# Optimization experiments

Hardware: AMD Instinct MI355X
Metric: run time of the kernel (lower is better)

## Reference

```python
import jax, jax.numpy as jnp
import numpy as np

EMBED_DIM = 1024
NUM_HEADS = 16
D_K = EMBED_DIM // NUM_HEADS
GAMMA = 1.0


def setup_inputs() -> dict:
    key = jax.random.key(0)
    ks = jax.random.split(key, 6)
    B, S, E = 4, 2048, EMBED_DIM
    scale = 1.0 / np.sqrt(E)
    x = jax.random.normal(ks[0], (B, S, E), dtype=jnp.float32)
    mask = jax.random.randint(ks[1], (B, S), 0, 2, dtype=jnp.int32)
    Wq = jax.random.normal(ks[2], (E, E), dtype=jnp.float32) * scale
    Wk = jax.random.normal(ks[3], (E, E), dtype=jnp.float32) * scale
    Wv = jax.random.normal(ks[4], (E, E), dtype=jnp.float32) * scale
    Wo = jax.random.normal(ks[5], (E, E), dtype=jnp.float32) * scale
    return {"x": x, "mask": mask, "Wq": Wq, "Wk": Wk, "Wv": Wv, "Wo": Wo}


def reference(x, mask, Wq, Wk, Wv, Wo):
    B, S, E = x.shape
    H, Dk = NUM_HEADS, D_K
    # projections (nn.Linear: y = x @ W.T), split heads -> [B, H, S, Dk]
    def proj(W):
        return (x @ W.T).reshape(B, S, H, Dk).transpose(0, 2, 1, 3)
    q = proj(Wq)
    k = proj(Wk)
    v = proj(Wv)
    # RBF kernel scores: exp(-gamma * ||q_i - k_j||^2)
    q_norm = jnp.sum(q * q, axis=-1, keepdims=True)            # [B,H,S,1]
    k_norm = jnp.sum(k * k, axis=-1, keepdims=True)            # [B,H,S,1]
    qk = jnp.einsum('bhsd,bhtd->bhst', q, k)                   # [B,H,S,S]
    dist_sq = q_norm + jnp.swapaxes(k_norm, -2, -1) - 2.0 * qk
    attn = jnp.exp(-GAMMA * dist_sq)
    # mask over keys: [B,1,1,S]
    attn = jnp.where(mask[:, None, None, :] == 0, 0.0, attn)
    # dropout is identity in eval mode
    out = jnp.einsum('bhst,bhtd->bhsd', attn, v)               # [B,H,S,Dk]
    out = out.transpose(0, 2, 1, 3).reshape(B, S, E)
    return out @ Wo.T
```

## Files before the change

kernel.cpp:

```cpp
#include <hip/hip_runtime.h>
#include <hip/hip_bf16.h>
#include <cstdint>
#include <cstddef>

#define B_ 4
#define S_ 2048
#define E_ 1024
#define H_ 16
#define BS_ (B_*S_)
#define BHS_ (B_*H_*S_)
#define MAXCAND (1u<<18)
#define SLOTS 512

static constexpr float T_SEARCH = 50.0f;
static constexpr float T_CUT    = 48.5f;

typedef __attribute__((ext_vector_type(8))) short bf16x8;
typedef __attribute__((ext_vector_type(4))) float f32x4;

static __device__ __forceinline__ unsigned short f32_to_bf16(float f){
  unsigned u = __float_as_uint(f);
  return (unsigned short)((u + 0x7fffu + ((u >> 16) & 1u)) >> 16);
}
static __device__ __forceinline__ void gload_lds16(const void* g, void* l){
  __builtin_amdgcn_global_load_lds(
      (const __attribute__((address_space(1))) unsigned int*)g,
      (__attribute__((address_space(3))) unsigned int*)l, 16, 0, 0);
}
static __device__ __forceinline__ float dot4(float4 a, float4 b){
  return a.x*b.x + a.y*b.y + a.z*b.z + a.w*b.w;
}

#define VMW(N_) asm volatile("s_waitcnt vmcnt(" #N_ ")" ::: "memory")
#define BAR()  do{ __builtin_amdgcn_s_barrier(); __builtin_amdgcn_sched_barrier(0); }while(0)

__global__ void cast_compact_k(const float* __restrict__ x,
                               const float* __restrict__ wq, const float* __restrict__ wk,
                               const int* __restrict__ mask,
                               unsigned short* __restrict__ xb, unsigned short* __restrict__ wqkb,
                               int* __restrict__ tmap, int* __restrict__ vcount){
  int blk = blockIdx.x;
  if (blk >= 5120){
    int b = blk - 5120, tid = threadIdx.x;
    __shared__ int ps[256];
    int loc[8]; int cnt = 0;
    #pragma unroll
    for (int j = 0; j < 8; ++j){ int m = mask[b*S_ + tid*8 + j]; loc[j] = m; cnt += m; }
    ps[tid] = cnt; __syncthreads();
    for (int off = 1; off < 256; off <<= 1){
      int v = (tid >= off) ? ps[tid-off] : 0;
      __syncthreads(); ps[tid] += v; __syncthreads();
    }
    int base = ps[tid] - cnt;
    #pragma unroll
    for (int j = 0; j < 8; ++j)
      if (loc[j]){ tmap[b*S_ + base] = tid*8 + j; ++base; }
    if (tid == 255) vcount[b] = ps[255];
    return;
  }
  const float* src; unsigned short* dst; int base;
  if (blk < 4096){ src = x;  dst = xb;                  base = blk; }
  else if (blk < 4608){ src = wq; dst = wqkb;           base = blk - 4096; }
  else { src = wk; dst = wqkb + (size_t)E_*E_;          base = blk - 4608; }
  size_t i = (size_t)base*256 + threadIdx.x;
  const float4* s4 = reinterpret_cast<const float4*>(src) + 2*i;
  float4 a = s4[0], b = s4[1];
  float v[8] = {a.x,a.y,a.z,a.w,b.x,b.y,b.z,b.w};
  union { unsigned short us[8]; uint4 u4; } o;
  #pragma unroll
  for (int j = 0; j < 8; ++j) o.us[j] = f32_to_bf16(v[j]);
  reinterpret_cast<uint4*>(dst)[i] = o.u4;
}

#define PROJ_STAGE(buf_, k0_) do{                                              \
  _Pragma("unroll") for (int i_ = 0; i_ < 4; ++i_){                            \
    int r_  = wave*32 + i_*8 + srow;                                           \
    int cs_ = sc ^ (r_ & 7);                                                   \
    gload_lds16(xb + ((size_t)(bb << 11) + arow[i_])*1024 + (k0_) + cs_*8,     \
                &At[buf_][(wave*32 + i_*8)*64]);                               \
    gload_lds16(Bw + (size_t)(n0 + r_)*1024 + (k0_) + cs_*8,                   \
                &Bt[buf_][(wave*32 + i_*8)*64]);                               \
  }                                                                            \
}while(0)

#define PROJ_COMPUTE(buf_) do{                                                 \
  _Pragma("unroll") for (int kk = 0; kk < 2; ++kk){                            \
    bf16x8 af[4], bf_[4];                                                      \
    _Pragma("unroll") for (int mf = 0; mf < 4; ++mf){                          \
      int r = wr*64 + mf*16 + fr;                                              \
      af[mf] = *reinterpret_cast<const bf16x8*>(                               \
          &At[buf_][r*64 + ((kk*4 + fc) ^ (r & 7))*8]);                        \
    }                                                                          \
    _Pragma("unroll") for (int nf = 0; nf < 4; ++nf){                          \
      int r = wc*64 + nf*16 + fr;                                              \
      bf_[nf] = *reinterpret_cast<const bf16x8*>(                              \
          &Bt[buf_][r*64 + ((kk*4 + fc) ^ (r & 7))*8]);                        \
    }                                                                          \
    _Pragma("unroll") for (int mf = 0; mf < 4; ++mf)                           \
    _Pragma("unroll") for (int nf = 0; nf < 4; ++nf)                           \
      acc[mf][nf] = __builtin_amdgcn_mfma_f32_16x16x32_bf16(                   \
          af[mf], bf_[nf], acc[mf][nf], 0, 0, 0);                              \
  }                                                                            \
}while(0)

__global__ __launch_bounds__(256) void proj_hm_k(
    const unsigned short* __restrict__ xb,
    const unsigned short* __restrict__ Wqkb,
    const int* __restrict__ tmap, const int* __restrict__ vcount,
    unsigned short* __restrict__ Qhm, unsigned short* __restrict__ Kc,
    float* __restrict__ qn, float* __restrict__ knc){
  const int z = blockIdx.z;
  const int m0 = blockIdx.x * 128, n0 = blockIdx.y * 128;
  const int bb = m0 >> 11, tc0 = m0 & 2047;
  const int vc = vcount[bb];
  if (z == 1 && tc0 >= vc) return;
  const unsigned short* Bw = Wqkb + (size_t)z*E_*E_;
  unsigned short* Out = z ? Kc : Qhm;
  float* Nrm = z ? knc : qn;

  __shared__ unsigned short At[2][128*64];
  __shared__ unsigned short Bt[2][128*64];
  const int tid = threadIdx.x, wave = tid >> 6, lane = tid & 63;
  const int wr = wave >> 1, wc = wave & 1;
  const int fr = lane & 15, fc = lane >> 4;
  const int srow = lane >> 3, sc = lane & 7;

  int arow[4];
  #pragma unroll
  for (int i = 0; i < 4; ++i){
    int r = wave*32 + i*8 + srow;
    int tc = tc0 + r;
    arow[i] = z ? ((tc < vc) ? tmap[bb*S_ + tc] : 0) : tc;
  }

  f32x4 acc[4][4] = {};

  PROJ_STAGE(0, 0);
  PROJ_STAGE(1, 64);
  VMW(8); BAR();
  #pragma unroll 2
  for (int t = 0; t < 16; ++t){
    PROJ_COMPUTE(t & 1);
    BAR();
    if (t + 2 < 16){
      PROJ_STAGE(t & 1, (t + 2)*64);
      VMW(8); BAR();
    } else if (t + 1 < 16){
      VMW(0); BAR();
    }
  }

  const int h = (n0 >> 6) + wc;
  const size_t rowbase = (size_t)((bb << 4) | h)*S_;
  #pragma unroll
  for (int mf = 0; mf < 4; ++mf)
    #pragma unroll
    for (int r = 0; r < 4; ++r){
      int rowb = tc0 + wr*64 + mf*16 + fc*4 + r;
      #pragma unroll
      for (int nf = 0; nf < 4; ++nf)
        Out[(rowbase + rowb)*64 + nf*16 + fr] = f32_to_bf16(acc[mf][nf][r]);
      float s = 0.f;
      #pragma unroll
      for (int nf = 0; nf < 4; ++nf) s += acc[mf][nf][r]*acc[mf][nf][r];
      s += __shfl_xor(s, 1); s += __shfl_xor(s, 2);
      s += __shfl_xor(s, 4); s += __shfl_xor(s, 8);
      if (fr == 0) Nrm[rowbase + rowb] = s;
    }
}

#define STAGE_K(slot_, c_) do{                                                 \
  _Pragma("unroll") for (int j_ = 0; j_ < 2; ++j_){                            \
    int rr_ = wave*16 + j_*8 + srow;                                           \
    gload_lds16(Kh + (size_t)((c_)*64 + rr_)*64 + (sc ^ (rr_ & 7))*8,          \
                &Kt[slot_][(wave*16 + j_*8)*64]);                              \
  }                                                                            \
}while(0)

#define TESTCHUNK(slot_, c_) do{                                               \
  int t0_ = (c_)*64;                                                           \
  bf16x8 af_[2], bfr_[4][2]; float knh_[4];                                    \
  { int r_ = wave*16 + fr;                                                     \
    _Pragma("unroll") for (int kk_ = 0; kk_ < 2; ++kk_)                        \
      af_[kk_] = *reinterpret_cast<const bf16x8*>(                             \
          &Qt[r_*64 + (((kk_*4 + fc) ^ (r_ & 7))*8)]); }                       \
  _Pragma("unroll") for (int nf_ = 0; nf_ < 4; ++nf_){                         \
    int tl_ = nf_*16 + fr;                                                     \
    _Pragma("unroll") for (int kk_ = 0; kk_ < 2; ++kk_)                        \
      bfr_[nf_][kk_] = *reinterpret_cast<const bf16x8*>(                       \
          &Kt[slot_][tl_*64 + (((kk_*4 + fc) ^ (tl_ & 7))*8)]);                \
    int t_ = t0_ + tl_;                                                        \
    knh_[nf_] = (t_ < vc) ? 0.5f*knl[t_] : 1e30f;                              \
  }                                                                            \
  f32x4 acc[4];                                                                \
  _Pragma("unroll") for (int nf_ = 0; nf_ < 4; ++nf_){                         \
    acc[nf_] = __builtin_amdgcn_mfma_f32_16x16x32_bf16(                        \
        af_[0], bfr_[nf_][0], z4, 0, 0, 0);                                    \
    acc[nf_] = __builtin_amdgcn_mfma_f32_16x16x32_bf16(                        \
        af_[1], bfr_[nf_][1], acc[nf_], 0, 0, 0);                              \
  }                                                                            \
  int hit_ = 0;                                                                \
  _Pragma("unroll") for (int nf_ = 0; nf_ < 4; ++nf_)                          \
  _Pragma("unroll") for (int r_ = 0; r_ < 4; ++r_)                             \
    hit_ |= (acc[nf_][r_] > qa[r_] + knh_[nf_]) ? 1 : 0;                       \
  if (__any(hit_)) hitmask |= (1u << (c_));                                    \
}while(0)

#define EMITCHUNK(c_) do{                                                      \
  int t0_ = (c_)*64;                                                           \
  bf16x8 af_[2], bfr_[4][2]; float knh_[4];                                    \
  { int r_ = wave*16 + fr;                                                     \
    _Pragma("unroll") for (int kk_ = 0; kk_ < 2; ++kk_)                        \
      af_[kk_] = *reinterpret_cast<const bf16x8*>(                             \
          &Qt[r_*64 + (((kk_*4 + fc) ^ (r_ & 7))*8)]); }                       \
  _Pragma("unroll") for (int nf_ = 0; nf_ < 4; ++nf_){                         \
    int tl_ = nf_*16 + fr;                                                     \
    _Pragma("unroll") for (int kk_ = 0; kk_ < 2; ++kk_)                        \
      bfr_[nf_][kk_] = *reinterpret_cast<const bf16x8*>(                       \
          Kh + (size_t)(t0_ + tl_)*64 + (kk_*4 + fc)*8);                       \
    int t_ = t0_ + tl_;                                                        \
    knh_[nf_] = (t_ < vc) ? 0.5f*knl[t_] : 1e30f;                              \
  }                                                                            \
  f32x4 acc[4];                                                                \
  _Pragma("unroll") for (int nf_ = 0; nf_ < 4; ++nf_){                         \
    acc[nf_] = __builtin_amdgcn_mfma_f32_16x16x32_bf16(                        \
        af_[0], bfr_[nf_][0], z4, 0, 0, 0);                                    \
    acc[nf_] = __builtin_amdgcn_mfma_f32_16x16x32_bf16(                        \
        af_[1], bfr_[nf_][1], acc[nf_], 0, 0, 0);                              \
  }                                                                            \
  _Pragma("unroll") for (int nf_ = 0; nf_ < 4; ++nf_)                          \
  _Pragma("unroll") for (int r_ = 0; r_ < 4; ++r_){                            \
    if (acc[nf_][r_] > qa[r_] + knh_[nf_]){                                    \
      int t_ = t0_ + nf_*16 + fr;                                              \
      if (t_ < vc){                                                            \
        int s_ = s0 + wave*16 + fc*4 + r_;                                     \
        unsigned idx_ = atomicAdd(cnt, 1u);                                    \
        if (idx_ < MAXCAND)                                                    \
          cand[idx_] = ((unsigned)b << 26) | ((unsigned)h << 22)               \
                     | ((unsigned)s_ << 11) | (unsigned)t_;                    \
        int qi_ = (bh << 11) | s_;                                             \
        if (atomicCAS((unsigned*)&qslotm[qi_], 0u, 1u) == 0u){                 \
          int sl_ = atomicAdd(&lcnt[h], 1);                                    \
          if (sl_ < SLOTS){                                                    \
            qlist[h*SLOTS + sl_] = (b << 11) | s_;                             \
            float4 zz_ = {0.f,0.f,0.f,0.f};                                    \
            float4* dz_ = reinterpret_cast<float4*>(                           \
                qex + (size_t)(h*SLOTS + sl_)*64);                             \
            for (int jz_ = 0; jz_ < 16; ++jz_) dz_[jz_] = zz_;                 \
            qslotm[qi_] = sl_ + 2;                                             \
          }                                                                    \
        }                                                                      \
        int ki_ = (bh << 11) | t_;                                             \
        if (atomicCAS((unsigned*)&kslotm[ki_], 0u, 1u) == 0u){                 \
          int sl_ = atomicAdd(&lcnt[16 + h], 1);                               \
          if (sl_ < SLOTS){                                                    \
            klist[h*SLOTS + sl_] = (b << 11) | t_;                             \
            float4 zz_ = {0.f,0.f,0.f,0.f};                                    \
            float4* d0_ = reinterpret_cast<float4*>(                           \
                kex + (size_t)(h*SLOTS + sl_)*64);                             \
            float4* d1_ = reinterpret_cast<float4*>(                           \
                vex + (size_t)(h*SLOTS + sl_)*64);                             \
            for (int jz_ = 0; jz_ < 16; ++jz_){ d0_[jz_] = zz_; d1_[jz_] = zz_; } \
            kslotm[ki_] = sl_ + 2;                                             \
          }                                                                    \
        }                                                                      \
      }                                                                        \
    }                                                                          \
  }                                                                            \
}while(0)

__global__ __launch_bounds__(256) void search_k(
    const unsigned short* __restrict__ Qhm, const unsigned short* __restrict__ Kc,
    const float* __restrict__ qn, const float* __restrict__ knc,
    const int* __restrict__ vcount,
    unsigned* __restrict__ cnt, unsigned* __restrict__ cand,
    int* __restrict__ lcnt, int* __restrict__ qlist, int* __restrict__ klist,
    int* __restrict__ qslotm, int* __restrict__ kslotm,
    float* __restrict__ qex, float* __restrict__ kex, float* __restrict__ vex){
  __shared__ unsigned short Qt[64*64];
  __shared__ unsigned short Kt[3][64*64];
  __shared__ float knl[S_];
  const int wave = threadIdx.x >> 6, lane = threadIdx.x & 63;
  const int bh = blockIdx.x & 63;
  const int s0 = (blockIdx.x >> 6) * 64;
  const int b = bh >> 4, h = bh & 15;
  const int vc = vcount[b];
  const int nt = (vc + 63) >> 6;
  if (nt == 0) return;
  const int fr = lane & 15, fc = lane >> 4;
  const int srow = lane >> 3, sc = lane & 7;
  const unsigned short* Qh = Qhm + (size_t)bh*S_*64;
  const unsigned short* Kh = Kc + (size_t)bh*S_*64;
  const float* qnb = qn + (size_t)bh*S_;
  const float* knb = knc + (size_t)bh*S_;
  const f32x4 z4 = {0.f, 0.f, 0.f, 0.f};

  float qa[4];
  #pragma unroll
  for (int r = 0; r < 4; ++r)
    qa[r] = 0.5f*(qnb[s0 + wave*16 + fc*4 + r] - T_SEARCH);
  float qamin = fminf(fminf(qa[0], qa[1]), fminf(qa[2], qa[3]));
  asm volatile("" :: "v"(qamin));
  asm volatile("s_waitcnt vmcnt(0)" ::: "memory");
  __builtin_amdgcn_sched_barrier(0);

  #pragma unroll
  for (int i = 0; i < 2; ++i){
    int r = wave*16 + i*8 + srow;
    gload_lds16(Qh + (size_t)(s0 + r)*64 + (sc ^ (r & 7))*8, &Qt[(wave*16 + i*8)*64]);
  }
  gload_lds16(knb + wave*512 + lane*4,       &knl[wave*512]);
  gload_lds16(knb + wave*512 + 256 + lane*4, &knl[wave*512 + 256]);
  STAGE_K(0, 0);
  if (nt > 1) STAGE_K(1, 1);

  unsigned hitmask = 0u;
  int c = 0, sl = 0;
  for (; c + 2 < nt; ++c){
    VMW(2); BAR();
    int sl2 = sl + 2; if (sl2 >= 3) sl2 -= 3;
    STAGE_K(sl2, c + 2);
    TESTCHUNK(sl, c);
    ++sl; if (sl == 3) sl = 0;
  }
  if (c + 1 < nt){ VMW(2); BAR(); TESTCHUNK(sl, c); ++c; ++sl; if (sl == 3) sl = 0; }
  VMW(0); BAR(); TESTCHUNK(sl, c);

  while (hitmask){
    int cc = __builtin_ctz(hitmask);
    hitmask &= hitmask - 1u;
    EMITCHUNK(cc);
  }
}

__global__ __launch_bounds__(256) void exact_rows_k(
    const float* __restrict__ x, const int* __restrict__ tmap,
    const float* __restrict__ Wq, const float* __restrict__ Wk,
    const float* __restrict__ Wv,
    const int* __restrict__ lcnt,
    const int* __restrict__ qlist, const int* __restrict__ klist,
    float* __restrict__ qex, float* __restrict__ kex, float* __restrict__ vex){
  int p = blockIdx.x, h = blockIdx.y, z = blockIdx.z;
  int R = lcnt[(z == 0 ? 0 : 16) + h]; if (R > SLOTS) R = SLOTS;
  if (R == 0) return;
  const float* W = (z == 0) ? Wq : (z == 1 ? Wk : Wv);
  const int* list = (z == 0) ? qlist : klist;
  float* dst = (z == 0) ? qex : (z == 1 ? kex : vex);
  int d = threadIdx.x >> 2, j = threadIdx.x & 3;
  const float4* w4 = reinterpret_cast<const float4*>(W + (size_t)(h*64 + d)*E_ + p*64 + j*16);
  float4 wa = w4[0], wb = w4[1], wcv = w4[2], wd = w4[3];
  for (int r = 0; r < R; ++r){
    int e = list[h*SLOTS + r];
    int b = e >> 11, rr = e & 2047;
    int row = (z == 0) ? rr : tmap[b*S_ + rr];
    const float4* x4 = reinterpret_cast<const float4*>(x + (size_t)(b*S_ + row)*E_ + p*64 + j*16);
    float acc = dot4(x4[0], wa) + dot4(x4[1], wb) + dot4(x4[2], wcv) + dot4(x4[3], wd);
    acc += __shfl_xor(acc, 1);
    acc += __shfl_xor(acc, 2);
    if (j == 0) atomicAdd(&dst[(size_t)(h*SLOTS + r)*64 + d], acc);
  }
}

__global__ __launch_bounds__(256) void d2scatter_k(
    const unsigned* __restrict__ cnt, const unsigned* __restrict__ cand,
    const int* __restrict__ qslotm, const int* __restrict__ kslotm,
    const float* __restrict__ qex, const float* __restrict__ kex,
    const float* __restrict__ vex, const float* __restrict__ Wo,
    float* __restrict__ out){
  unsigned n = *cnt; if (n > MAXCAND) n = MAXCAND;
  int lane = threadIdx.x & 63;
  for (unsigned i = blockIdx.x; i < n; i += gridDim.x){
    unsigned u = cand[i];
    int b = (int)(u >> 26), h = (int)((u >> 22) & 15);
    int s = (int)((u >> 11) & 2047), tc = (int)(u & 2047);
    int qi = ((b*16 + h) << 11) | s, ki = ((b*16 + h) << 11) | tc;
    int qs = qslotm[qi] - 2, ks = kslotm[ki] - 2;
    float sq;
    if (qs >= 0 && ks >= 0){
      float a = qex[(size_t)(h*SLOTS + qs)*64 + lane] - kex[(size_t)(h*SLOTS + ks)*64 + lane];
      sq = a*a;
    } else sq = 1e30f;
    #pragma unroll
    for (int o = 32; o; o >>= 1) sq += __shfl_xor(sq, o);
    if (sq >= T_CUT) continue;
    float w = expf(-sq);
    const float4* vv4 = reinterpret_cast<const float4*>(vex + (size_t)(h*SLOTS + ks)*64);
    #pragma unroll
    for (int c4 = 0; c4 < 4; ++c4){
      int e = c4*256 + threadIdx.x;
      const float4* wo4 = reinterpret_cast<const float4*>(Wo + (size_t)e*E_ + h*64);
      float a = 0.f;
      #pragma unroll
      for (int d2 = 0; d2 < 16; ++d2){
        float4 vv = vv4[d2], ww = wo4[d2];
        a += vv.x*ww.x + vv.y*ww.y + vv.z*ww.z + vv.w*ww.w;
      }
      atomicAdd(&out[(size_t)(b*S_ + s)*E_ + e], w*a);
    }
  }
}

extern "C" void kernel_launch(void* const* d_in, const int* in_sizes, int n_in,
                              void* d_out, int out_size, void* d_ws, size_t ws_size,
                              hipStream_t stream){
  const float* x  = (const float*)d_in[0];
  const int* mask = (const int*)d_in[1];
  const float* Wq = (const float*)d_in[2];
  const float* Wk = (const float*)d_in[3];
  const float* Wv = (const float*)d_in[4];
  const float* Wo = (const float*)d_in[5];
  float* out = (float*)d_out;

  char* w = (char*)d_ws;
  unsigned short* Qhm = (unsigned short*)w; w += (size_t)BS_*E_*2;
  unsigned short* Kc  = (unsigned short*)w; w += (size_t)BS_*E_*2;
  unsigned short* xb  = (unsigned short*)w; w += (size_t)BS_*E_*2;
  unsigned short* Wqkb = (unsigned short*)w; w += (size_t)E_*E_*2*2;
  float* qn  = (float*)w; w += (size_t)BHS_*4;
  float* knc = (float*)w; w += (size_t)BHS_*4;
  int* tmap   = (int*)w; w += (size_t)BS_*4;
  int* vcount = (int*)w; w += 256;
  unsigned* cand = (unsigned*)w; w += (size_t)MAXCAND*4;
  int* qlist  = (int*)w; w += (size_t)H_*SLOTS*4;
  int* klist  = (int*)w; w += (size_t)H_*SLOTS*4;
  float* qex = (float*)w; w += (size_t)H_*SLOTS*64*4;
  float* kex = (float*)w; w += (size_t)H_*SLOTS*64*4;
  float* vex = (float*)w; w += (size_t)H_*SLOTS*64*4;
  char* zbase = w;
  unsigned* cnt  = (unsigned*)w; w += 256;
  int* lcnt = (int*)w; w += 256;
  int* qslotm = (int*)w; w += (size_t)BHS_*4;
  int* kslotm = (int*)w; w += (size_t)BHS_*4;
  size_t zbytes = (size_t)(w - zbase);

  hipMemsetAsync(d_out, 0, (size_t)out_size*sizeof(float), stream);
  hipMemsetAsync(zbase, 0, zbytes, stream);

  cast_compact_k<<<5124, 256, 0, stream>>>(x, Wq, Wk, mask, xb, Wqkb, tmap, vcount);

  proj_hm_k<<<dim3(64, 8, 2), 256, 0, stream>>>(xb, Wqkb, tmap, vcount, Qhm, Kc, qn, knc);

  search_k<<<32*64, 256, 0, stream>>>(Qhm, Kc, qn, knc, vcount, cnt, cand,
                                      lcnt, qlist, klist, qslotm, kslotm, qex, kex, vex);

  exact_rows_k<<<dim3(16, 16, 3), 256, 0, stream>>>(x, tmap, Wq, Wk, Wv, lcnt, qlist, klist, qex, kex, vex);
  d2scatter_k<<<512, 256, 0, stream>>>(cnt, cand, qslotm, kslotm, qex, kex, vex, Wo, out);
}
```

Baseline: 164.0 us.

## Fuse output zeroing into cast kernel and hoist Q fragments in search loop

Replaces the separate memset of the output buffer with extra blocks in the cast/compact kernel that write zeros, removing one launch. In the search kernel, Q fragments are loaded from LDS once into registers instead of per chunk. Out-of-range key norms are pre-filled with a large sentinel in LDS, so the per-element validity check in the test and emit paths can be dropped. The chunk loop is also unrolled by three with constant ring-buffer slots. These cut per-chunk LDS reads and index arithmetic at the cost of more register pressure.

```diff
diff --git a/kernel.cpp b/kernel.cpp
--- a/kernel.cpp
+++ b/kernel.cpp
@@ -38,8 +38,18 @@
                                const float* __restrict__ wq, const float* __restrict__ wk,
                                const int* __restrict__ mask,
                                unsigned short* __restrict__ xb, unsigned short* __restrict__ wqkb,
-                               int* __restrict__ tmap, int* __restrict__ vcount){
+                               int* __restrict__ tmap, int* __restrict__ vcount,
+                               float* __restrict__ outz){
   int blk = blockIdx.x;
+  if (blk >= 5124){
+    float4* f4 = reinterpret_cast<float4*>(outz + (size_t)(blk - 5124)*4096);
+    float4 z = {0.f,0.f,0.f,0.f};
+    f4[threadIdx.x]       = z;
+    f4[threadIdx.x + 256] = z;
+    f4[threadIdx.x + 512] = z;
+    f4[threadIdx.x + 768] = z;
+    return;
+  }
   if (blk >= 5120){
     int b = blk - 5120, tid = threadIdx.x;
     __shared__ int ps[256];
@@ -179,25 +189,20 @@
 
 #define TESTCHUNK(slot_, c_) do{                                               \
   int t0_ = (c_)*64;                                                           \
-  bf16x8 af_[2], bfr_[4][2]; float knh_[4];                                    \
-  { int r_ = wave*16 + fr;                                                     \
-    _Pragma("unroll") for (int kk_ = 0; kk_ < 2; ++kk_)                        \
-      af_[kk_] = *reinterpret_cast<const bf16x8*>(                             \
-          &Qt[r_*64 + (((kk_*4 + fc) ^ (r_ & 7))*8)]); }                       \
+  bf16x8 bfr_[4][2]; float knh_[4];                                            \
   _Pragma("unroll") for (int nf_ = 0; nf_ < 4; ++nf_){                         \
     int tl_ = nf_*16 + fr;                                                     \
     _Pragma("unroll") for (int kk_ = 0; kk_ < 2; ++kk_)                        \
       bfr_[nf_][kk_] = *reinterpret_cast<const bf16x8*>(                       \
           &Kt[slot_][tl_*64 + (((kk_*4 + fc) ^ (tl_ & 7))*8)]);                \
-    int t_ = t0_ + tl_;                                                        \
-    knh_[nf_] = (t_ < vc) ? 0.5f*knl[t_] : 1e30f;                              \
+    knh_[nf_] = 0.5f*knl[t0_ + tl_];                                           \
   }                                                                            \
   f32x4 acc[4];                                                                \
   _Pragma("unroll") for (int nf_ = 0; nf_ < 4; ++nf_){                         \
     acc[nf_] = __builtin_amdgcn_mfma_f32_16x16x32_bf16(                        \
-        af_[0], bfr_[nf_][0], z4, 0, 0, 0);                                    \
+        afh[0], bfr_[nf_][0], z4, 0, 0, 0);                                    \
     acc[nf_] = __builtin_amdgcn_mfma_f32_16x16x32_bf16(                        \
-        af_[1], bfr_[nf_][1], acc[nf_], 0, 0, 0);                              \
+        afh[1], bfr_[nf_][1], acc[nf_], 0, 0, 0);                              \
   }                                                                            \
   int hit_ = 0;                                                                \
   _Pragma("unroll") for (int nf_ = 0; nf_ < 4; ++nf_)                          \
@@ -208,61 +213,54 @@
 
 #define EMITCHUNK(c_) do{                                                      \
   int t0_ = (c_)*64;                                                           \
-  bf16x8 af_[2], bfr_[4][2]; float knh_[4];                                    \
-  { int r_ = wave*16 + fr;                                                     \
-    _Pragma("unroll") for (int kk_ = 0; kk_ < 2; ++kk_)                        \
-      af_[kk_] = *reinterpret_cast<const bf16x8*>(                             \
-          &Qt[r_*64 + (((kk_*4 + fc) ^ (r_ & 7))*8)]); }                       \
+  bf16x8 bfr_[4][2]; float knh_[4];                                            \
   _Pragma("unroll") for (int nf_ = 0; nf_ < 4; ++nf_){                         \
     int tl_ = nf_*16 + fr;                                                     \
     _Pragma("unroll") for (int kk_ = 0; kk_ < 2; ++kk_)                        \
       bfr_[nf_][kk_] = *reinterpret_cast<const bf16x8*>(                       \
           Kh + (size_t)(t0_ + tl_)*64 + (kk_*4 + fc)*8);                       \
-    int t_ = t0_ + tl_;                                                        \
-    knh_[nf_] = (t_ < vc) ? 0.5f*knl[t_] : 1e30f;                              \
+    knh_[nf_] = 0.5f*knl[t0_ + tl_];                                           \
   }                                                                            \
   f32x4 acc[4];                                                                \
   _Pragma("unroll") for (int nf_ = 0; nf_ < 4; ++nf_){                         \
     acc[nf_] = __builtin_amdgcn_mfma_f32_16x16x32_bf16(                        \
-        af_[0], bfr_[nf_][0], z4, 0, 0, 0);                                    \
+        afh[0], bfr_[nf_][0], z4, 0, 0, 0);                                    \
     acc[nf_] = __builtin_amdgcn_mfma_f32_16x16x32_bf16(                        \
-        af_[1], bfr_[nf_][1], acc[nf_], 0, 0, 0);                              \
+        afh[1], bfr_[nf_][1], acc[nf_], 0, 0, 0);                              \
   }                                                                            \
   _Pragma("unroll") for (int nf_ = 0; nf_ < 4; ++nf_)                          \
   _Pragma("unroll") for (int r_ = 0; r_ < 4; ++r_){                            \
     if (acc[nf_][r_] > qa[r_] + knh_[nf_]){                                    \
       int t_ = t0_ + nf_*16 + fr;                                              \
-      if (t_ < vc){                                                            \
-        int s_ = s0 + wave*16 + fc*4 + r_;                                     \
-        unsigned idx_ = atomicAdd(cnt, 1u);                                    \
-        if (idx_ < MAXCAND)                                                    \
-          cand[idx_] = ((unsigned)b << 26) | ((unsigned)h << 22)               \
-                     | ((unsigned)s_ << 11) | (unsigned)t_;                    \
-        int qi_ = (bh << 11) | s_;                                             \
-        if (atomicCAS((unsigned*)&qslotm[qi_], 0u, 1u) == 0u){                 \
-          int sl_ = atomicAdd(&lcnt[h], 1);                                    \
-          if (sl_ < SLOTS){                                                    \
-            qlist[h*SLOTS + sl_] = (b << 11) | s_;                             \
-            float4 zz_ = {0.f,0.f,0.f,0.f};                                    \
-            float4* dz_ = reinterpret_cast<float4*>(                           \
-                qex + (size_t)(h*SLOTS + sl_)*64);                             \
-            for (int jz_ = 0; jz_ < 16; ++jz_) dz_[jz_] = zz_;                 \
-            qslotm[qi_] = sl_ + 2;                                             \
-          }                                                                    \
+      int s_ = s0 + wave*16 + fc*4 + r_;                                       \
+      unsigned idx_ = atomicAdd(cnt, 1u);                                      \
+      if (idx_ < MAXCAND)                                                      \
+        cand[idx_] = ((unsigned)b << 26) | ((unsigned)h << 22)                 \
+                   | ((unsigned)s_ << 11) | (unsigned)t_;                      \
+      int qi_ = (bh << 11) | s_;                                               \
+      if (atomicCAS((unsigned*)&qslotm[qi_], 0u, 1u) == 0u){                   \
+        int sl_ = atomicAdd(&lcnt[h], 1);                                      \
+        if (sl_ < SLOTS){                                                      \
+          qlist[h*SLOTS + sl_] = (b << 11) | s_;                               \
+          float4 zz_ = {0.f,0.f,0.f,0.f};                                      \
+          float4* dz_ = reinterpret_cast<float4*>(                             \
+              qex + (size_t)(h*SLOTS + sl_)*64);                               \
+          for (int jz_ = 0; jz_ < 16; ++jz_) dz_[jz_] = zz_;                   \
+          qslotm[qi_] = sl_ + 2;                                               \
         }                                                                      \
-        int ki_ = (bh << 11) | t_;                                             \
-        if (atomicCAS((unsigned*)&kslotm[ki_], 0u, 1u) == 0u){                 \
-          int sl_ = atomicAdd(&lcnt[16 + h], 1);                               \
-          if (sl_ < SLOTS){                                                    \
-            klist[h*SLOTS + sl_] = (b << 11) | t_;                             \
-            float4 zz_ = {0.f,0.f,0.f,0.f};                                    \
-            float4* d0_ = reinterpret_cast<float4*>(                           \
-                kex + (size_t)(h*SLOTS + sl_)*64);                             \
-            float4* d1_ = reinterpret_cast<float4*>(                           \
-                vex + (size_t)(h*SLOTS + sl_)*64);                             \
-            for (int jz_ = 0; jz_ < 16; ++jz_){ d0_[jz_] = zz_; d1_[jz_] = zz_; } \
-            kslotm[ki_] = sl_ + 2;                                             \
-          }                                                                    \
+      }                                                                        \
+      int ki_ = (bh << 11) | t_;                                               \
+      if (atomicCAS((unsigned*)&kslotm[ki_], 0u, 1u) == 0u){                   \
+        int sl_ = atomicAdd(&lcnt[16 + h], 1);                                 \
+        if (sl_ < SLOTS){                                                      \
+          klist[h*SLOTS + sl_] = (b << 11) | t_;                               \
+          float4 zz_ = {0.f,0.f,0.f,0.f};                                      \
+          float4* d0_ = reinterpret_cast<float4*>(                             \
+              kex + (size_t)(h*SLOTS + sl_)*64);                               \
+          float4* d1_ = reinterpret_cast<float4*>(                             \
+              vex + (size_t)(h*SLOTS + sl_)*64);                               \
+          for (int jz_ = 0; jz_ < 16; ++jz_){ d0_[jz_] = zz_; d1_[jz_] = zz_; } \
+          kslotm[ki_] = sl_ + 2;                                               \
         }                                                                      \
       }                                                                        \
     }                                                                          \
@@ -314,8 +312,29 @@
   STAGE_K(0, 0);
   if (nt > 1) STAGE_K(1, 1);
 
+  VMW(4);
+  bf16x8 afh[2];
+  { int r_ = wave*16 + fr;
+    #pragma unroll
+    for (int kk = 0; kk < 2; ++kk)
+      afh[kk] = *reinterpret_cast<const bf16x8*>(&Qt[r_*64 + (((kk*4 + fc) ^ (r_ & 7))*8)]);
+  }
+  { int lo = vc > wave*512 ? vc : wave*512;
+    int hi = nt*64 < (wave+1)*512 ? nt*64 : (wave+1)*512;
+    for (int t = lo + lane; t < hi; t += 64) knl[t] = 1e30f;
+  }
+  asm volatile("s_waitcnt lgkmcnt(0)" ::: "memory");
+  __builtin_amdgcn_sched_barrier(0);
+
   unsigned hitmask = 0u;
-  int c = 0, sl = 0;
+  int c = 0;
+  while (c + 4 < nt){
+    VMW(2); BAR(); STAGE_K(2, c + 2); TESTCHUNK(0, c);
+    VMW(2); BAR(); STAGE_K(0, c + 3); TESTCHUNK(1, c + 1);
+    VMW(2); BAR(); STAGE_K(1, c + 4); TESTCHUNK(2, c + 2);
+    c += 3;
+  }
+  int sl = c - (c/3)*3;
   for (; c + 2 < nt; ++c){
     VMW(2); BAR();
     int sl2 = sl + 2; if (sl2 >= 3) sl2 -= 3;
@@ -433,10 +452,9 @@
   int* kslotm = (int*)w; w += (size_t)BHS_*4;
   size_t zbytes = (size_t)(w - zbase);
 
-  hipMemsetAsync(d_out, 0, (size_t)out_size*sizeof(float), stream);
   hipMemsetAsync(zbase, 0, zbytes, stream);
 
-  cast_compact_k<<<5124, 256, 0, stream>>>(x, Wq, Wk, mask, xb, Wqkb, tmap, vcount);
+  cast_compact_k<<<5124 + 2048, 256, 0, stream>>>(x, Wq, Wk, mask, xb, Wqkb, tmap, vcount, out);
 
   proj_hm_k<<<dim3(64, 8, 2), 256, 0, stream>>>(xb, Wqkb, tmap, vcount, Qhm, Kc, qn, knc);
 
```

Result: faster. 157.6 us (-3.9%).
